# Kernel tuning notes

Hardware: AMD Instinct MI355X
Metric: run time of the kernel (lower is better)

The kernel has to match this reference:

```python
import jax, jax.numpy as jnp
import numpy as np

N = 50000      # areaNum
E = 64         # embeddingsize
NE = 800000    # nonzeros of normalized adjacency
WK = 9         # walk_length + 1
L = 2          # args.L
TMP = 0.5      # args.choosing_tmp
BIAS = 1e-4


def _logistic_noise(k, shape):
    # eps ~ U(bias, 1-bias); noise = log(eps) - log(1-eps)
    u = jax.random.uniform(k, shape, minval=BIAS, maxval=1.0 - BIAS)
    return jnp.log(u) - jnp.log1p(-u)


def setup_inputs() -> dict:
    key = jax.random.key(0)
    ks = jax.random.split(key, 16)
    rng = np.random.default_rng(0)

    # ---- normalized sparse adjacency (D^-1/2 A D^-1/2), COO sorted by row ----
    row = np.sort(rng.integers(0, N, NE))
    col = rng.integers(0, N, NE)
    deg = np.bincount(row, minlength=N).astype(np.float32)
    dinv = np.where(deg > 0, deg ** -0.5, 0.0).astype(np.float32)
    vals = dinv[row] * dinv[col]

    # ---- random-walk mean-pooling adjacency, row-normalized ----
    rw_row = np.repeat(np.arange(N), WK)
    rw_col = rng.integers(0, N, N * WK)
    rw_col[::WK] = np.arange(N)  # walk starts at self
    rw_vals = np.full(N * WK, 1.0 / WK, dtype=np.float32)

    def lin(k, fan_in, shape):
        return jax.random.normal(k, shape, dtype=jnp.float32) / np.sqrt(fan_in)

    inp = {
        'x': jax.random.normal(ks[0], (N, E), dtype=jnp.float32),
        'vals': jnp.asarray(vals),
        'rw_vals': jnp.asarray(rw_vals),
        't_W1': lin(ks[1], 2 * E, (L, 2 * E, E)),
        't_b1': jnp.zeros((L, E), jnp.float32),
        't_W2': lin(ks[2], E, (L, E, 1)),
        't_b2': jnp.zeros((L, 1), jnp.float32),
        's_W1': lin(ks[3], E, (L, E, E)),
        's_b1': jnp.zeros((L, E), jnp.float32),
        's_W2': lin(ks[4], E, (L, E, 1)),
        's_b2': jnp.zeros((L, 1), jnp.float32),
        't_noise': _logistic_noise(ks[5], (L, NE)),
        's_noise': _logistic_noise(ks[6], (L, N, 1)),
        'row': jnp.asarray(row, dtype=jnp.int64) if jax.config.jax_enable_x64 else jnp.asarray(row, dtype=jnp.int32),
        'col': jnp.asarray(col, dtype=jnp.int32),
        'rw_row': jnp.asarray(rw_row, dtype=jnp.int32),
        'rw_col': jnp.asarray(rw_col, dtype=jnp.int32),
    }
    inp['row'] = jnp.asarray(row, dtype=jnp.int32)
    return inp


def reference(x, vals, rw_vals, t_W1, t_b1, t_W2, t_b2, s_W1, s_b1, s_W2, s_b2,
              t_noise, s_noise, row, col, rw_row, rw_col):
    n = x.shape[0]

    def spmm(r, c, v, h):  # sparse [n,n] @ dense [n,E]
        return jax.ops.segment_sum(v[:, None] * h[c], r, num_segments=n)

    # per-edge concat of ORIGINAL embeddings (same tensor every layer, as in source)
    t_cat = jnp.concatenate([x[row], x[col]], axis=-1)  # [nE, 2E]

    # --- mask-learning pass ---
    cur = x
    t_masks, s_masks = [], []
    for i in range(L):
        cur = spmm(row, col, vals, cur)
        t_h = jax.nn.relu(t_cat @ t_W1[i] + t_b1[i])
        t_logit = t_h @ t_W2[i] + t_b2[i]                      # [nE,1]
        t_m = jax.nn.sigmoid((t_noise[i][:, None] + t_logit) / TMP)[:, 0]
        t_masks.append(t_m)
        s_h = jax.nn.relu(cur @ s_W1[i] + s_b1[i])
        s_logit = s_h @ s_W2[i] + s_b2[i]                      # [N,1]
        s_masks.append(jax.nn.sigmoid((s_noise[i] + s_logit) / TMP))

    # --- t branch: gated spmm propagation, mean over layers ---
    cur_t = x
    acc_t = x
    for i in range(L):
        cur_t = spmm(row, col, vals * t_masks[i], cur_t)
        acc_t = acc_t + cur_t
    emb_t = acc_t / (L + 1)

    # --- s branch: gated mix with random-walk mean pooling, then spmm ---
    cur_s = x
    acc_s = x
    s_reg = jnp.float32(0.0)
    for i in range(L):
        mp = spmm(rw_row, rw_col, rw_vals, cur_s)
        cur_s = s_masks[i] * cur_s + (1.0 - s_masks[i]) * mp
        cur_s = spmm(row, col, vals, cur_s)
        acc_s = acc_s + cur_s
        s_reg = s_reg + s_masks[i].sum() / n
    emb_s = acc_s / (L + 1)
    s_reg = s_reg / L
    t_reg = jnp.float32(0.0)  # source never accumulates into t_reg
    return emb_t, emb_s, t_reg, s_reg, t_masks[-1]
```

## Files before the change

### kernel.cpp

```cpp
#include <hip/hip_runtime.h>

#define NNODES 50000
#define EDIM 64
#define WKLEN 9
#define NEDGE 800000
#define NPAD (NNODES + 64)

#define NGRP 6250
#define GSTRIDE 1250

using bf16x8 = __attribute__((ext_vector_type(8))) __bf16;
using f32x4  = __attribute__((ext_vector_type(4))) float;

__device__ __align__(256) unsigned short g_xbf[NPAD * EDIM];
__device__ __align__(256) unsigned short g_ABh[NNODES * 128];
__device__ __align__(256) unsigned short g_c1h[NPAD * EDIM];
__device__ __align__(256) unsigned short g_c2h[NPAD * EDIM];
__device__ __align__(256) unsigned short g_g0h[NNODES * EDIM];
__device__ __align__(256) unsigned short g_sc1h[NNODES * EDIM];
__device__ __align__(256) unsigned short g_Pr[NNODES * 128];
__device__ __align__(256) unsigned short g_Pc[NNODES * 128];
__device__ __align__(256) float g_mt0[NEDGE];
__device__ __align__(256) float g_mt1[NEDGE];
__device__ __align__(256) float g_sm0[NNODES];
__device__ __align__(256) float g_sm1[NNODES];
__device__ __align__(256) int   g_rowptr[NNODES + 1];
__device__ __align__(256) unsigned short g_Tswz[2048 * 8];
__device__ __align__(256) unsigned short g_Sswz[1024 * 8];

__device__ __forceinline__ unsigned short f2bf(float f) {
    union { float f; unsigned int i; } v;
    v.f = f;
    unsigned int r = v.i + 0x7FFFu + ((v.i >> 16) & 1u);
    return (unsigned short)(r >> 16);
}
__device__ __forceinline__ float bf2f_lo(unsigned int u) {
    union { unsigned int i; float f; } v; v.i = u << 16; return v.f;
}
__device__ __forceinline__ float bf2f_hi(unsigned int u) {
    union { unsigned int i; float f; } v; v.i = u & 0xFFFF0000u; return v.f;
}

__global__ __launch_bounds__(256) void misc_kernel(
    const float* __restrict__ x, const float* __restrict__ tW1,
    const float* __restrict__ sW1, const int* __restrict__ row,
    int n, int nE)
{
    int bid = blockIdx.x, tid = threadIdx.x;
    if (bid < 1563) {
        int i = bid * 256 + tid;
        if (i < NNODES * EDIM / 8) {
            const float* src = x + i * 8;
            union { unsigned short s[8]; uint4 q; } u;
#pragma unroll
            for (int j = 0; j < 8; ++j) u.s[j] = f2bf(src[j]);
            *(uint4*)&g_xbf[i * 8] = u.q;
        }
    } else if (bid < 1759) {
        int i = (bid - 1563) * 256 + tid;
        if (i > n) return;
        int lo = 0, hi = nE;
        while (lo < hi) {
            int mid = (lo + hi) >> 1;
            if (row[mid] < i) lo = mid + 1; else hi = mid;
        }
        g_rowptr[i] = lo;
    } else if (bid < 1767) {
        int t = (bid - 1759) * 256 + tid;
        int s = t >> 9, f = (t >> 6) & 7, ln = t & 63;
        int li = s >> 1, half = s & 1, ks = f >> 2, nn = f & 3;
        int q = ln >> 4, mcl = ln & 15;
        union { unsigned short sv[8]; uint4 q4; } u;
#pragma unroll
        for (int j = 0; j < 8; ++j) {
            int kg = half * 64 + ks * 32 + q * 8 + j;
            u.sv[j] = f2bf(tW1[li * 8192 + kg * 64 + nn * 16 + mcl]);
        }
        *(uint4*)&g_Tswz[t * 8] = u.q4;
    } else {
        int t = (bid - 1767) * 256 + tid;
        int li = t >> 9, ks = (t >> 8) & 1, nn = (t >> 6) & 3, ln = t & 63;
        int q = ln >> 4, mcl = ln & 15;
        union { unsigned short sv[8]; uint4 q4; } u;
#pragma unroll
        for (int j = 0; j < 8; ++j)
            u.sv[j] = f2bf(sW1[li * 4096 + (ks * 32 + q * 8 + j) * 64 + nn * 16 + mcl]);
        *(uint4*)&g_Sswz[t * 8] = u.q4;
    }
}

__global__ __launch_bounds__(256) void prep2_kernel(int n)
{
    int tid = threadIdx.x;
    int wave = tid >> 6, lane = tid & 63;
    int mc = lane & 15, quad = lane >> 4;
    int nb = blockIdx.x * 64 + wave * 16;
    const unsigned short* bp = g_xbf + (nb + mc) * 64 + quad * 8;
    bf16x8 af0 = *(const bf16x8*)bp;
    bf16x8 af1 = *(const bf16x8*)(bp + 32);
    const f32x4 zero = {0.f, 0.f, 0.f, 0.f};
#pragma unroll
    for (int s = 0; s < 4; ++s) {
        int li = s >> 1, half = s & 1;
        f32x4 acc[4];
#pragma unroll
        for (int nn = 0; nn < 4; ++nn) acc[nn] = zero;
#pragma unroll
        for (int nn = 0; nn < 4; ++nn) {
            bf16x8 b0 = *(const bf16x8*)&g_Tswz[((s * 8 + nn) * 64 + lane) * 8];
            bf16x8 b1 = *(const bf16x8*)&g_Tswz[((s * 8 + 4 + nn) * 64 + lane) * 8];
            acc[nn] = __builtin_amdgcn_mfma_f32_16x16x32_bf16(af0, b0, acc[nn], 0, 0, 0);
            acc[nn] = __builtin_amdgcn_mfma_f32_16x16x32_bf16(af1, b1, acc[nn], 0, 0, 0);
        }
        unsigned short* dst = half ? g_Pc : g_Pr;
#pragma unroll
        for (int nn = 0; nn < 4; ++nn)
#pragma unroll
            for (int r = 0; r < 4; ++r) {
                int node = nb + quad * 4 + r;
                if (node < n)
                    dst[node * 128 + li * 64 + nn * 16 + mc] = f2bf(acc[nn][r]);
            }
    }
}

__global__ __launch_bounds__(256) void edge_mask_kernel(
    const float* __restrict__ tb1, const float* __restrict__ tW2,
    const float* __restrict__ tb2, const float* __restrict__ tnoise,
    const int* __restrict__ row, const int* __restrict__ col,
    float* __restrict__ mask_out, int nE)
{
    int tid = threadIdx.x;
    int lane = tid & 63;
    int sub = lane & 7;
    int eg = lane >> 3;

    float b1_0[8], b1_1[8], w2_0[8], w2_1[8];
    *(float4*)&b1_0[0] = *(const float4*)&tb1[sub * 8];
    *(float4*)&b1_0[4] = *(const float4*)&tb1[sub * 8 + 4];
    *(float4*)&b1_1[0] = *(const float4*)&tb1[64 + sub * 8];
    *(float4*)&b1_1[4] = *(const float4*)&tb1[64 + sub * 8 + 4];
    *(float4*)&w2_0[0] = *(const float4*)&tW2[sub * 8];
    *(float4*)&w2_0[4] = *(const float4*)&tW2[sub * 8 + 4];
    *(float4*)&w2_1[0] = *(const float4*)&tW2[64 + sub * 8];
    *(float4*)&w2_1[4] = *(const float4*)&tW2[64 + sub * 8 + 4];
    float tb2_0 = tb2[0], tb2_1 = tb2[1];

    int nvb = nE / 32;
    for (int vb = blockIdx.x; vb < nvb; vb += GSTRIDE) {
        int wv = vb * 4 + (tid >> 6);
        int e = wv * 8 + eg;

        int rn = row[e], cn = col[e];
        uint4 qr0 = *(const uint4*)&g_Pr[rn * 128 + sub * 8];
        uint4 qr1 = *(const uint4*)&g_Pr[rn * 128 + 64 + sub * 8];
        uint4 qc0 = *(const uint4*)&g_Pc[cn * 128 + sub * 8];
        uint4 qc1 = *(const uint4*)&g_Pc[cn * 128 + 64 + sub * 8];

        float p0 = 0.f, p1 = 0.f;
        unsigned r0[4] = {qr0.x, qr0.y, qr0.z, qr0.w};
        unsigned r1[4] = {qr1.x, qr1.y, qr1.z, qr1.w};
        unsigned c0[4] = {qc0.x, qc0.y, qc0.z, qc0.w};
        unsigned c1[4] = {qc1.x, qc1.y, qc1.z, qc1.w};
#pragma unroll
        for (int k = 0; k < 4; ++k) {
            float hA = fmaxf(bf2f_lo(r0[k]) + bf2f_lo(c0[k]) + b1_0[2 * k], 0.f);
            float hB = fmaxf(bf2f_hi(r0[k]) + bf2f_hi(c0[k]) + b1_0[2 * k + 1], 0.f);
            p0 = fmaf(hA, w2_0[2 * k], p0);
            p0 = fmaf(hB, w2_0[2 * k + 1], p0);
            float gA = fmaxf(bf2f_lo(r1[k]) + bf2f_lo(c1[k]) + b1_1[2 * k], 0.f);
            float gB = fmaxf(bf2f_hi(r1[k]) + bf2f_hi(c1[k]) + b1_1[2 * k + 1], 0.f);
            p1 = fmaf(gA, w2_1[2 * k], p1);
            p1 = fmaf(gB, w2_1[2 * k + 1], p1);
        }
#pragma unroll
        for (int off = 1; off <= 4; off <<= 1) {
            p0 += __shfl_xor(p0, off, 64);
            p1 += __shfl_xor(p1, off, 64);
        }
        if (sub == 0) {
            float z0 = (tnoise[e] + p0 + tb2_0) * 2.0f;
            float m0 = 1.0f / (1.0f + expf(-z0));
            g_mt0[e] = m0;
            float z1 = (tnoise[nE + e] + p1 + tb2_1) * 2.0f;
            float m1 = 1.0f / (1.0f + expf(-z1));
            g_mt1[e] = m1;
            mask_out[e] = m1;
        }
    }
}

__device__ __forceinline__ void nm_body(
    int bid, const unsigned short* __restrict__ cur, int li,
    const float* __restrict__ b1, const float* __restrict__ W2,
    const float* __restrict__ b2, const float* __restrict__ noise,
    float* __restrict__ smout, int n)
{
    int tid = threadIdx.x;
    int wave = tid >> 6, lane = tid & 63;
    int mc = lane & 15, quad = lane >> 4;
    int nb = bid * 64 + wave * 16;
    const unsigned short* basep = cur + (nb + mc) * 64 + quad * 8;
    bf16x8 af0 = *(const bf16x8*)basep;
    bf16x8 af1 = *(const bf16x8*)(basep + 32);
    f32x4 acc[4];
    const f32x4 zero = {0.f, 0.f, 0.f, 0.f};
#pragma unroll
    for (int nn = 0; nn < 4; ++nn) acc[nn] = zero;
#pragma unroll
    for (int nn = 0; nn < 4; ++nn) {
        bf16x8 b0 = *(const bf16x8*)&g_Sswz[((li * 8 + nn) * 64 + lane) * 8];
        bf16x8 b1f = *(const bf16x8*)&g_Sswz[((li * 8 + 4 + nn) * 64 + lane) * 8];
        acc[nn] = __builtin_amdgcn_mfma_f32_16x16x32_bf16(af0, b0, acc[nn], 0, 0, 0);
        acc[nn] = __builtin_amdgcn_mfma_f32_16x16x32_bf16(af1, b1f, acc[nn], 0, 0, 0);
    }
    float p[4];
#pragma unroll
    for (int r = 0; r < 4; ++r) {
        float s = 0.f;
#pragma unroll
        for (int nn = 0; nn < 4; ++nn) {
            float h = acc[nn][r] + b1[nn * 16 + mc];
            s = fmaf(fmaxf(h, 0.f), W2[nn * 16 + mc], s);
        }
        p[r] = s;
    }
#pragma unroll
    for (int off = 8; off >= 1; off >>= 1)
#pragma unroll
        for (int r = 0; r < 4; ++r) p[r] += __shfl_xor(p[r], off, 64);
    if (mc == 0) {
        float b2v = b2[0];
#pragma unroll
        for (int r = 0; r < 4; ++r) {
            int node = nb + quad * 4 + r;
            if (node < n) {
                float z = (noise[node] + p[r] + b2v) * 2.0f;
                smout[node] = 1.0f / (1.0f + expf(-z));
            }
        }
    }
}

__global__ __launch_bounds__(256) void nm0_kernel(
    const float* __restrict__ sb1, const float* __restrict__ sW2,
    const float* __restrict__ sb2, const float* __restrict__ snz, int n)
{
    nm_body(blockIdx.x, g_c1h, 0, sb1, sW2, sb2, snz, g_sm0, n);
}

__device__ __forceinline__ void s1_process16(
    int sb, int d2, int myc, float myv, float myvm,
    float& p0, float& p1, float& q0, float& q1)
{
    int cc[16]; float vv[16], mm[16]; unsigned uu[16];
#pragma unroll
    for (int k = 0; k < 16; ++k) {
        cc[k] = __shfl(myc, sb + k, 64);
        vv[k] = __shfl(myv, sb + k, 64);
        mm[k] = __shfl(myvm, sb + k, 64);
    }
#pragma unroll
    for (int k = 0; k < 16; ++k)
        uu[k] = *(const unsigned*)&g_xbf[cc[k] * 64 + 2 * d2];
#pragma unroll
    for (int k = 0; k < 16; ++k) {
        p0 = fmaf(vv[k], bf2f_lo(uu[k]), p0);
        p1 = fmaf(vv[k], bf2f_hi(uu[k]), p1);
        q0 = fmaf(mm[k], bf2f_lo(uu[k]), q0);
        q1 = fmaf(mm[k], bf2f_hi(uu[k]), q1);
    }
}

__global__ __launch_bounds__(256) void s1_kernel(
    const int* __restrict__ colv, const float* __restrict__ vals, int n)
{
    int half = threadIdx.x >> 5;
    int el = half & 1;
    int d2 = threadIdx.x & 31;
    int sb0 = el << 5;
    for (int rb = blockIdx.x; rb < NGRP; rb += GSTRIDE) {
        int w = rb * 8 + half;
        int s = g_rowptr[w], e = g_rowptr[w + 1];
        float p0 = 0.f, p1 = 0.f, q0 = 0.f, q1 = 0.f;
        for (int base = s; base < e; base += 32) {
            int rem = e - base;
            int myc = 0; float myv = 0.f, myvm = 0.f;
            if (d2 < rem) {
                myc = colv[base + d2];
                myv = vals[base + d2];
                myvm = myv * g_mt0[base + d2];
            }
            s1_process16(sb0, d2, myc, myv, myvm, p0, p1, q0, q1);
            if (rem > 16)
                s1_process16(sb0 + 16, d2, myc, myv, myvm, p0, p1, q0, q1);
        }
        uint2 pk;
        pk.x = (unsigned)f2bf(p0) | ((unsigned)f2bf(q0) << 16);
        pk.y = (unsigned)f2bf(p1) | ((unsigned)f2bf(q1) << 16);
        *(uint2*)&g_ABh[w * 128 + 4 * d2] = pk;
        *(unsigned*)&g_c1h[w * 64 + 2 * d2] =
            (unsigned)f2bf(p0) | ((unsigned)f2bf(p1) << 16);
    }
}

__device__ __forceinline__ void s2_process8(
    int sb, int d2, int myc, float myv, float myvm,
    float& c0, float& c1, float& t0, float& t1)
{
    int cc[8]; float vv[8], mm[8]; uint2 uu[8];
#pragma unroll
    for (int k = 0; k < 8; ++k) {
        cc[k] = __shfl(myc, sb + k, 64);
        vv[k] = __shfl(myv, sb + k, 64);
        mm[k] = __shfl(myvm, sb + k, 64);
    }
#pragma unroll
    for (int k = 0; k < 8; ++k)
        uu[k] = *(const uint2*)&g_ABh[cc[k] * 128 + 4 * d2];
#pragma unroll
    for (int k = 0; k < 8; ++k) {
        c0 = fmaf(vv[k], bf2f_lo(uu[k].x), c0);
        t0 = fmaf(mm[k], bf2f_hi(uu[k].x), t0);
        c1 = fmaf(vv[k], bf2f_lo(uu[k].y), c1);
        t1 = fmaf(mm[k], bf2f_hi(uu[k].y), t1);
    }
}

__device__ __forceinline__ void rw_body(
    int bid, const int* __restrict__ rw_col, const float* __restrict__ rwv,
    const unsigned short* __restrict__ cur, const float* __restrict__ smask,
    unsigned short* __restrict__ outg)
{
    int w = bid * 8 + (threadIdx.x >> 5);
    int d2 = threadIdx.x & 31;
    int base = w * WKLEN;
    float a0 = 0.f, a1 = 0.f;
#pragma unroll
    for (int j = 0; j < WKLEN; ++j) {
        int c = rw_col[base + j];
        float v = rwv[base + j];
        unsigned u = *(const unsigned*)&cur[c * 64 + 2 * d2];
        a0 = fmaf(v, bf2f_lo(u), a0);
        a1 = fmaf(v, bf2f_hi(u), a1);
    }
    float sm = smask[w];
    unsigned u = *(const unsigned*)&cur[w * 64 + 2 * d2];
    float r0 = sm * bf2f_lo(u) + (1.f - sm) * a0;
    float r1 = sm * bf2f_hi(u) + (1.f - sm) * a1;
    *(unsigned*)&outg[w * 64 + 2 * d2] =
        (unsigned)f2bf(r0) | ((unsigned)f2bf(r1) << 16);
}

__global__ __launch_bounds__(256) void s2_rw0_kernel(
    const int* __restrict__ colv, const float* __restrict__ vals,
    const int* __restrict__ rw_col, const float* __restrict__ rwv,
    const float* __restrict__ x, float* __restrict__ emb_t, int n)
{
    int half = threadIdx.x >> 5;
    int el = half & 1;
    int d2 = threadIdx.x & 31;
    int sb0 = el << 5;
    for (int vb = blockIdx.x; vb < 2 * NGRP; vb += GSTRIDE) {
        if (vb >= NGRP) {
            rw_body(vb - NGRP, rw_col, rwv, g_xbf, g_sm0, g_g0h);
            continue;
        }
        int w = vb * 8 + half;
        int s = g_rowptr[w], e = g_rowptr[w + 1];
        float c0 = 0.f, c1 = 0.f, t0 = 0.f, t1 = 0.f;
        for (int base = s; base < e; base += 32) {
            int rem = e - base;
            int myc = 0; float myv = 0.f, myvm = 0.f;
            if (d2 < rem) {
                myc = colv[base + d2];
                myv = vals[base + d2];
                myvm = myv * g_mt1[base + d2];
            }
            s2_process8(sb0, d2, myc, myv, myvm, c0, c1, t0, t1);
            if (rem > 8)  s2_process8(sb0 + 8,  d2, myc, myv, myvm, c0, c1, t0, t1);
            if (rem > 16) s2_process8(sb0 + 16, d2, myc, myv, myvm, c0, c1, t0, t1);
            if (rem > 24) s2_process8(sb0 + 24, d2, myc, myv, myvm, c0, c1, t0, t1);
        }
        int o2 = w * 64 + 2 * d2;
        uint2 U2v = *(const uint2*)&g_ABh[w * 128 + 4 * d2];
        float2 et;
        et.x = (x[o2]     + bf2f_hi(U2v.x) + t0) * (1.0f / 3.0f);
        et.y = (x[o2 + 1] + bf2f_hi(U2v.y) + t1) * (1.0f / 3.0f);
        *(float2*)&emb_t[o2] = et;
        *(unsigned*)&g_c2h[o2] = (unsigned)f2bf(c0) | ((unsigned)f2bf(c1) << 16);
    }
}

__device__ __forceinline__ void sp_process16(
    const unsigned short* __restrict__ h, int sb, int d2,
    int myc, float myv, float& a0, float& a1)
{
    int cc[16]; float vv[16]; unsigned uu[16];
#pragma unroll
    for (int k = 0; k < 16; ++k) {
        cc[k] = __shfl(myc, sb + k, 64);
        vv[k] = __shfl(myv, sb + k, 64);
    }
#pragma unroll
    for (int k = 0; k < 16; ++k)
        uu[k] = *(const unsigned*)&h[cc[k] * 64 + 2 * d2];
#pragma unroll
    for (int k = 0; k < 16; ++k) {
        a0 = fmaf(vv[k], bf2f_lo(uu[k]), a0);
        a1 = fmaf(vv[k], bf2f_hi(uu[k]), a1);
    }
}

__device__ __forceinline__ void spmm_body(
    int bid, const int* __restrict__ colv, const float* __restrict__ vals,
    const unsigned short* __restrict__ h, float* __restrict__ l0,
    float* __restrict__ l1, int* __restrict__ wout, int* __restrict__ d2out)
{
    int half = threadIdx.x >> 5;
    int w = bid * 8 + half;
    int el = half & 1;
    int d2 = threadIdx.x & 31;
    int sb0 = el << 5;
    int s = g_rowptr[w], e = g_rowptr[w + 1];
    float a0 = 0.f, a1 = 0.f;
    for (int base = s; base < e; base += 32) {
        int rem = e - base;
        int myc = 0; float myv = 0.f;
        if (d2 < rem) {
            myc = colv[base + d2];
            myv = vals[base + d2];
        }
        sp_process16(h, sb0, d2, myc, myv, a0, a1);
        if (rem > 16) sp_process16(h, sb0 + 16, d2, myc, myv, a0, a1);
    }
    *l0 = a0; *l1 = a1; *wout = w; *d2out = d2;
}

__global__ __launch_bounds__(256) void spmm10_nm1_kernel(
    const int* __restrict__ colv, const float* __restrict__ vals,
    const float* __restrict__ sb1, const float* __restrict__ sW2,
    const float* __restrict__ sb2, const float* __restrict__ snz, int n)
{
    for (int vb = blockIdx.x; vb < NGRP + 782; vb += GSTRIDE) {
        if (vb >= NGRP) {
            nm_body(vb - NGRP, g_c2h, 1, sb1, sW2, sb2, snz, g_sm1, n);
            continue;
        }
        float a0, a1; int w, d2;
        spmm_body(vb, colv, vals, g_g0h, &a0, &a1, &w, &d2);
        *(unsigned*)&g_sc1h[w * 64 + 2 * d2] =
            (unsigned)f2bf(a0) | ((unsigned)f2bf(a1) << 16);
    }
}

__global__ __launch_bounds__(256) void rw1_kernel(
    const int* __restrict__ rw_col, const float* __restrict__ rwv)
{
    for (int vb = blockIdx.x; vb < NGRP; vb += GSTRIDE)
        rw_body(vb, rw_col, rwv, g_sc1h, g_sm1, g_g0h);
}

__global__ __launch_bounds__(256) void spmm12_fin_kernel(
    const int* __restrict__ colv, const float* __restrict__ vals,
    const float* __restrict__ x, float* __restrict__ emb_s,
    float* __restrict__ out, int n)
{
    if (blockIdx.x >= GSTRIDE) {
        __shared__ float red[256];
        float s = 0.f;
        for (int i = threadIdx.x; i < n; i += 256) s += g_sm0[i] + g_sm1[i];
        red[threadIdx.x] = s;
        __syncthreads();
        for (int off = 128; off >= 1; off >>= 1) {
            if (threadIdx.x < off) red[threadIdx.x] += red[threadIdx.x + off];
            __syncthreads();
        }
        if (threadIdx.x == 0) {
            out[6400000] = 0.0f;
            out[6400001] = red[0] / (2.0f * n);
        }
        return;
    }
    for (int vb = blockIdx.x; vb < NGRP; vb += GSTRIDE) {
        float a0, a1; int w, d2;
        spmm_body(vb, colv, vals, g_g0h, &a0, &a1, &w, &d2);
        int o2 = w * 64 + 2 * d2;
        unsigned uc = *(const unsigned*)&g_sc1h[o2];
        float2 es;
        es.x = (x[o2]     + bf2f_lo(uc) + a0) * (1.0f / 3.0f);
        es.y = (x[o2 + 1] + bf2f_hi(uc) + a1) * (1.0f / 3.0f);
        *(float2*)&emb_s[o2] = es;
    }
}

extern "C" void kernel_launch(void* const* d_in, const int* in_sizes, int n_in,
                              void* d_out, int out_size, void* d_ws, size_t ws_size,
                              hipStream_t stream)
{
    const float* x    = (const float*)d_in[0];
    const float* vals = (const float*)d_in[1];
    const float* rwv  = (const float*)d_in[2];
    const float* tW1  = (const float*)d_in[3];
    const float* tb1  = (const float*)d_in[4];
    const float* tW2  = (const float*)d_in[5];
    const float* tb2  = (const float*)d_in[6];
    const float* sW1  = (const float*)d_in[7];
    const float* sb1  = (const float*)d_in[8];
    const float* sW2  = (const float*)d_in[9];
    const float* sb2  = (const float*)d_in[10];
    const float* tnz  = (const float*)d_in[11];
    const float* snz  = (const float*)d_in[12];
    const int* row   = (const int*)d_in[13];
    const int* colv  = (const int*)d_in[14];
    const int* rwcol = (const int*)d_in[16];

    const int n = NNODES;
    const int nE = in_sizes[1];

    float* out   = (float*)d_out;
    float* emb_t = out;
    float* emb_s = out + 3200000;
    float* masko = out + 6400002;

    misc_kernel<<<1771, 256, 0, stream>>>(x, tW1, sW1, row, n, nE);
    prep2_kernel<<<782, 256, 0, stream>>>(n);
    edge_mask_kernel<<<GSTRIDE, 256, 0, stream>>>(tb1, tW2, tb2, tnz,
                                                  row, colv, masko, nE);
    s1_kernel<<<GSTRIDE, 256, 0, stream>>>(colv, vals, n);
    nm0_kernel<<<782, 256, 0, stream>>>(sb1, sW2, sb2, snz, n);
    s2_rw0_kernel<<<GSTRIDE, 256, 0, stream>>>(colv, vals, rwcol, rwv, x, emb_t, n);
    spmm10_nm1_kernel<<<GSTRIDE, 256, 0, stream>>>(colv, vals,
                                                   sb1 + 64, sW2 + 64, sb2 + 1,
                                                   snz + n, n);
    rw1_kernel<<<GSTRIDE, 256, 0, stream>>>(rwcol, rwv);
    spmm12_fin_kernel<<<GSTRIDE + 1, 256, 0, stream>>>(colv, vals, x, emb_s, out, n);
}
```

Before: 346.0 us.

## Remap sparse kernels to 16 lanes per row with wider vector gathers

Each row is now handled by 16 lanes instead of 32, and each lane covers 4 feature columns (8 in the packed pass) using uint2/uint4 loads. Before, edge indices were loaded once per lane and then broadcast with shuffles. Now every lane loads the edge indices and values directly, in unrolled batches of 16. Grid sizes change to match the new row grouping. The aim is fewer shuffle instructions and fewer, wider gather transactions per row, at the cost of redundant index loads and higher register pressure.

```diff
diff --git a/kernel.cpp b/kernel.cpp
--- a/kernel.cpp
+++ b/kernel.cpp
@@ -6,7 +6,9 @@
 #define NEDGE 800000
 #define NPAD (NNODES + 64)
 
-#define NGRP 6250
+#define NG16 3125
+#define GS1 1563
+#define GS2 1303
 #define GSTRIDE 1250
 
 using bf16x8 = __attribute__((ext_vector_type(8))) __bf16;
@@ -249,107 +251,89 @@
     nm_body(blockIdx.x, g_c1h, 0, sb1, sW2, sb2, snz, g_sm0, n);
 }
 
-__device__ __forceinline__ void s1_process16(
-    int sb, int d2, int myc, float myv, float myvm,
-    float& p0, float& p1, float& q0, float& q1)
-{
-    int cc[16]; float vv[16], mm[16]; unsigned uu[16];
-#pragma unroll
-    for (int k = 0; k < 16; ++k) {
-        cc[k] = __shfl(myc, sb + k, 64);
-        vv[k] = __shfl(myv, sb + k, 64);
-        mm[k] = __shfl(myvm, sb + k, 64);
-    }
-#pragma unroll
-    for (int k = 0; k < 16; ++k)
-        uu[k] = *(const unsigned*)&g_xbf[cc[k] * 64 + 2 * d2];
-#pragma unroll
-    for (int k = 0; k < 16; ++k) {
-        p0 = fmaf(vv[k], bf2f_lo(uu[k]), p0);
-        p1 = fmaf(vv[k], bf2f_hi(uu[k]), p1);
-        q0 = fmaf(mm[k], bf2f_lo(uu[k]), q0);
-        q1 = fmaf(mm[k], bf2f_hi(uu[k]), q1);
-    }
-}
-
 __global__ __launch_bounds__(256) void s1_kernel(
     const int* __restrict__ colv, const float* __restrict__ vals, int n)
 {
-    int half = threadIdx.x >> 5;
-    int el = half & 1;
-    int d2 = threadIdx.x & 31;
-    int sb0 = el << 5;
-    for (int rb = blockIdx.x; rb < NGRP; rb += GSTRIDE) {
-        int w = rb * 8 + half;
+    int g = threadIdx.x >> 4;
+    int l = threadIdx.x & 15;
+    for (int vb = blockIdx.x; vb < NG16; vb += GS1) {
+        int w = vb * 16 + g;
         int s = g_rowptr[w], e = g_rowptr[w + 1];
-        float p0 = 0.f, p1 = 0.f, q0 = 0.f, q1 = 0.f;
-        for (int base = s; base < e; base += 32) {
-            int rem = e - base;
-            int myc = 0; float myv = 0.f, myvm = 0.f;
-            if (d2 < rem) {
-                myc = colv[base + d2];
-                myv = vals[base + d2];
-                myvm = myv * g_mt0[base + d2];
+        float p0 = 0.f, p1 = 0.f, p2 = 0.f, p3 = 0.f;
+        float q0 = 0.f, q1 = 0.f, q2 = 0.f, q3 = 0.f;
+        for (int base = s; base < e; base += 16) {
+            int cc[16]; float vv[16], mm[16];
+#pragma unroll
+            for (int k = 0; k < 16; ++k) {
+                int idx = base + k;
+                bool ok = idx < e;
+                cc[k] = ok ? colv[idx] : 0;
+                float v = ok ? vals[idx] : 0.f;
+                vv[k] = v;
+                mm[k] = ok ? v * g_mt0[idx] : 0.f;
             }
-            s1_process16(sb0, d2, myc, myv, myvm, p0, p1, q0, q1);
-            if (rem > 16)
-                s1_process16(sb0 + 16, d2, myc, myv, myvm, p0, p1, q0, q1);
-        }
-        uint2 pk;
+            uint2 uu[16];
+#pragma unroll
+            for (int k = 0; k < 16; ++k)
+                uu[k] = *(const uint2*)&g_xbf[cc[k] * 64 + 4 * l];
+#pragma unroll
+            for (int k = 0; k < 16; ++k) {
+                p0 = fmaf(vv[k], bf2f_lo(uu[k].x), p0);
+                p1 = fmaf(vv[k], bf2f_hi(uu[k].x), p1);
+                p2 = fmaf(vv[k], bf2f_lo(uu[k].y), p2);
+                p3 = fmaf(vv[k], bf2f_hi(uu[k].y), p3);
+                q0 = fmaf(mm[k], bf2f_lo(uu[k].x), q0);
+                q1 = fmaf(mm[k], bf2f_hi(uu[k].x), q1);
+                q2 = fmaf(mm[k], bf2f_lo(uu[k].y), q2);
+                q3 = fmaf(mm[k], bf2f_hi(uu[k].y), q3);
+            }
+        }
+        uint4 pk;
         pk.x = (unsigned)f2bf(p0) | ((unsigned)f2bf(q0) << 16);
         pk.y = (unsigned)f2bf(p1) | ((unsigned)f2bf(q1) << 16);
-        *(uint2*)&g_ABh[w * 128 + 4 * d2] = pk;
-        *(unsigned*)&g_c1h[w * 64 + 2 * d2] =
-            (unsigned)f2bf(p0) | ((unsigned)f2bf(p1) << 16);
-    }
-}
-
-__device__ __forceinline__ void s2_process8(
-    int sb, int d2, int myc, float myv, float myvm,
-    float& c0, float& c1, float& t0, float& t1)
-{
-    int cc[8]; float vv[8], mm[8]; uint2 uu[8];
-#pragma unroll
-    for (int k = 0; k < 8; ++k) {
-        cc[k] = __shfl(myc, sb + k, 64);
-        vv[k] = __shfl(myv, sb + k, 64);
-        mm[k] = __shfl(myvm, sb + k, 64);
-    }
-#pragma unroll
-    for (int k = 0; k < 8; ++k)
-        uu[k] = *(const uint2*)&g_ABh[cc[k] * 128 + 4 * d2];
-#pragma unroll
-    for (int k = 0; k < 8; ++k) {
-        c0 = fmaf(vv[k], bf2f_lo(uu[k].x), c0);
-        t0 = fmaf(mm[k], bf2f_hi(uu[k].x), t0);
-        c1 = fmaf(vv[k], bf2f_lo(uu[k].y), c1);
-        t1 = fmaf(mm[k], bf2f_hi(uu[k].y), t1);
-    }
-}
-
-__device__ __forceinline__ void rw_body(
+        pk.z = (unsigned)f2bf(p2) | ((unsigned)f2bf(q2) << 16);
+        pk.w = (unsigned)f2bf(p3) | ((unsigned)f2bf(q3) << 16);
+        *(uint4*)&g_ABh[w * 128 + 8 * l] = pk;
+        uint2 ch;
+        ch.x = (unsigned)f2bf(p0) | ((unsigned)f2bf(p1) << 16);
+        ch.y = (unsigned)f2bf(p2) | ((unsigned)f2bf(p3) << 16);
+        *(uint2*)&g_c1h[w * 64 + 4 * l] = ch;
+    }
+}
+
+__device__ __forceinline__ void rw_body16(
     int bid, const int* __restrict__ rw_col, const float* __restrict__ rwv,
     const unsigned short* __restrict__ cur, const float* __restrict__ smask,
     unsigned short* __restrict__ outg)
 {
-    int w = bid * 8 + (threadIdx.x >> 5);
-    int d2 = threadIdx.x & 31;
+    int g = threadIdx.x >> 4, l = threadIdx.x & 15;
+    int w = bid * 16 + g;
     int base = w * WKLEN;
-    float a0 = 0.f, a1 = 0.f;
+    int cc[WKLEN]; float vv[WKLEN];
 #pragma unroll
     for (int j = 0; j < WKLEN; ++j) {
-        int c = rw_col[base + j];
-        float v = rwv[base + j];
-        unsigned u = *(const unsigned*)&cur[c * 64 + 2 * d2];
-        a0 = fmaf(v, bf2f_lo(u), a0);
-        a1 = fmaf(v, bf2f_hi(u), a1);
+        cc[j] = rw_col[base + j];
+        vv[j] = rwv[base + j];
+    }
+    float a0 = 0.f, a1 = 0.f, a2 = 0.f, a3 = 0.f;
+#pragma unroll
+    for (int j = 0; j < WKLEN; ++j) {
+        uint2 u = *(const uint2*)&cur[cc[j] * 64 + 4 * l];
+        a0 = fmaf(vv[j], bf2f_lo(u.x), a0);
+        a1 = fmaf(vv[j], bf2f_hi(u.x), a1);
+        a2 = fmaf(vv[j], bf2f_lo(u.y), a2);
+        a3 = fmaf(vv[j], bf2f_hi(u.y), a3);
     }
     float sm = smask[w];
-    unsigned u = *(const unsigned*)&cur[w * 64 + 2 * d2];
-    float r0 = sm * bf2f_lo(u) + (1.f - sm) * a0;
-    float r1 = sm * bf2f_hi(u) + (1.f - sm) * a1;
-    *(unsigned*)&outg[w * 64 + 2 * d2] =
-        (unsigned)f2bf(r0) | ((unsigned)f2bf(r1) << 16);
+    uint2 u = *(const uint2*)&cur[w * 64 + 4 * l];
+    float r0 = sm * bf2f_lo(u.x) + (1.f - sm) * a0;
+    float r1 = sm * bf2f_hi(u.x) + (1.f - sm) * a1;
+    float r2 = sm * bf2f_lo(u.y) + (1.f - sm) * a2;
+    float r3 = sm * bf2f_hi(u.y) + (1.f - sm) * a3;
+    uint2 o;
+    o.x = (unsigned)f2bf(r0) | ((unsigned)f2bf(r1) << 16);
+    o.y = (unsigned)f2bf(r2) | ((unsigned)f2bf(r3) << 16);
+    *(uint2*)&outg[w * 64 + 4 * l] = o;
 }
 
 __global__ __launch_bounds__(256) void s2_rw0_kernel(
@@ -357,84 +341,97 @@
     const int* __restrict__ rw_col, const float* __restrict__ rwv,
     const float* __restrict__ x, float* __restrict__ emb_t, int n)
 {
-    int half = threadIdx.x >> 5;
-    int el = half & 1;
-    int d2 = threadIdx.x & 31;
-    int sb0 = el << 5;
-    for (int vb = blockIdx.x; vb < 2 * NGRP; vb += GSTRIDE) {
-        if (vb >= NGRP) {
-            rw_body(vb - NGRP, rw_col, rwv, g_xbf, g_sm0, g_g0h);
+    int g = threadIdx.x >> 4;
+    int l = threadIdx.x & 15;
+    for (int vb = blockIdx.x; vb < 2 * NG16; vb += GS1) {
+        if (vb >= NG16) {
+            rw_body16(vb - NG16, rw_col, rwv, g_xbf, g_sm0, g_g0h);
             continue;
         }
-        int w = vb * 8 + half;
+        int w = vb * 16 + g;
         int s = g_rowptr[w], e = g_rowptr[w + 1];
-        float c0 = 0.f, c1 = 0.f, t0 = 0.f, t1 = 0.f;
-        for (int base = s; base < e; base += 32) {
-            int rem = e - base;
-            int myc = 0; float myv = 0.f, myvm = 0.f;
-            if (d2 < rem) {
-                myc = colv[base + d2];
-                myv = vals[base + d2];
-                myvm = myv * g_mt1[base + d2];
+        float c0 = 0.f, c1 = 0.f, c2 = 0.f, c3 = 0.f;
+        float t0 = 0.f, t1 = 0.f, t2 = 0.f, t3 = 0.f;
+        for (int base = s; base < e; base += 16) {
+            int cc[16]; float vv[16], mm[16];
+#pragma unroll
+            for (int k = 0; k < 16; ++k) {
+                int idx = base + k;
+                bool ok = idx < e;
+                cc[k] = ok ? colv[idx] : 0;
+                float v = ok ? vals[idx] : 0.f;
+                vv[k] = v;
+                mm[k] = ok ? v * g_mt1[idx] : 0.f;
             }
-            s2_process8(sb0, d2, myc, myv, myvm, c0, c1, t0, t1);
-            if (rem > 8)  s2_process8(sb0 + 8,  d2, myc, myv, myvm, c0, c1, t0, t1);
-            if (rem > 16) s2_process8(sb0 + 16, d2, myc, myv, myvm, c0, c1, t0, t1);
-            if (rem > 24) s2_process8(sb0 + 24, d2, myc, myv, myvm, c0, c1, t0, t1);
-        }
-        int o2 = w * 64 + 2 * d2;
-        uint2 U2v = *(const uint2*)&g_ABh[w * 128 + 4 * d2];
-        float2 et;
-        et.x = (x[o2]     + bf2f_hi(U2v.x) + t0) * (1.0f / 3.0f);
-        et.y = (x[o2 + 1] + bf2f_hi(U2v.y) + t1) * (1.0f / 3.0f);
-        *(float2*)&emb_t[o2] = et;
-        *(unsigned*)&g_c2h[o2] = (unsigned)f2bf(c0) | ((unsigned)f2bf(c1) << 16);
-    }
-}
-
-__device__ __forceinline__ void sp_process16(
-    const unsigned short* __restrict__ h, int sb, int d2,
-    int myc, float myv, float& a0, float& a1)
-{
-    int cc[16]; float vv[16]; unsigned uu[16];
-#pragma unroll
-    for (int k = 0; k < 16; ++k) {
-        cc[k] = __shfl(myc, sb + k, 64);
-        vv[k] = __shfl(myv, sb + k, 64);
-    }
-#pragma unroll
-    for (int k = 0; k < 16; ++k)
-        uu[k] = *(const unsigned*)&h[cc[k] * 64 + 2 * d2];
-#pragma unroll
-    for (int k = 0; k < 16; ++k) {
-        a0 = fmaf(vv[k], bf2f_lo(uu[k]), a0);
-        a1 = fmaf(vv[k], bf2f_hi(uu[k]), a1);
-    }
-}
-
-__device__ __forceinline__ void spmm_body(
-    int bid, const int* __restrict__ colv, const float* __restrict__ vals,
-    const unsigned short* __restrict__ h, float* __restrict__ l0,
-    float* __restrict__ l1, int* __restrict__ wout, int* __restrict__ d2out)
-{
-    int half = threadIdx.x >> 5;
-    int w = bid * 8 + half;
-    int el = half & 1;
-    int d2 = threadIdx.x & 31;
-    int sb0 = el << 5;
+#pragma unroll
+            for (int h = 0; h < 2; ++h) {
+                if (h == 1 && e - base <= 8) break;
+                uint4 uu[8];
+#pragma unroll
+                for (int k = 0; k < 8; ++k)
+                    uu[k] = *(const uint4*)&g_ABh[cc[h * 8 + k] * 128 + 8 * l];
+#pragma unroll
+                for (int k = 0; k < 8; ++k) {
+                    float v = vv[h * 8 + k], m = mm[h * 8 + k];
+                    c0 = fmaf(v, bf2f_lo(uu[k].x), c0);
+                    t0 = fmaf(m, bf2f_hi(uu[k].x), t0);
+                    c1 = fmaf(v, bf2f_lo(uu[k].y), c1);
+                    t1 = fmaf(m, bf2f_hi(uu[k].y), t1);
+                    c2 = fmaf(v, bf2f_lo(uu[k].z), c2);
+                    t2 = fmaf(m, bf2f_hi(uu[k].z), t2);
+                    c3 = fmaf(v, bf2f_lo(uu[k].w), c3);
+                    t3 = fmaf(m, bf2f_hi(uu[k].w), t3);
+                }
+            }
+        }
+        int o = w * 64 + 4 * l;
+        uint4 U = *(const uint4*)&g_ABh[w * 128 + 8 * l];
+        float4 xv = *(const float4*)&x[o];
+        float4 et;
+        et.x = (xv.x + bf2f_hi(U.x) + t0) * (1.0f / 3.0f);
+        et.y = (xv.y + bf2f_hi(U.y) + t1) * (1.0f / 3.0f);
+        et.z = (xv.z + bf2f_hi(U.z) + t2) * (1.0f / 3.0f);
+        et.w = (xv.w + bf2f_hi(U.w) + t3) * (1.0f / 3.0f);
+        *(float4*)&emb_t[o] = et;
+        uint2 ch;
+        ch.x = (unsigned)f2bf(c0) | ((unsigned)f2bf(c1) << 16);
+        ch.y = (unsigned)f2bf(c2) | ((unsigned)f2bf(c3) << 16);
+        *(uint2*)&g_c2h[o] = ch;
+    }
+}
+
+__device__ __forceinline__ void spmm_body16(
+    int vb, const int* __restrict__ colv, const float* __restrict__ vals,
+    const unsigned short* __restrict__ h,
+    float& a0, float& a1, float& a2, float& a3, int& wout, int& lout)
+{
+    int g = threadIdx.x >> 4;
+    int l = threadIdx.x & 15;
+    int w = vb * 16 + g;
     int s = g_rowptr[w], e = g_rowptr[w + 1];
-    float a0 = 0.f, a1 = 0.f;
-    for (int base = s; base < e; base += 32) {
-        int rem = e - base;
-        int myc = 0; float myv = 0.f;
-        if (d2 < rem) {
-            myc = colv[base + d2];
-            myv = vals[base + d2];
-        }
-        sp_process16(h, sb0, d2, myc, myv, a0, a1);
-        if (rem > 16) sp_process16(h, sb0 + 16, d2, myc, myv, a0, a1);
-    }
-    *l0 = a0; *l1 = a1; *wout = w; *d2out = d2;
+    a0 = a1 = a2 = a3 = 0.f;
+    for (int base = s; base < e; base += 16) {
+        int cc[16]; float vv[16];
+#pragma unroll
+        for (int k = 0; k < 16; ++k) {
+            int idx = base + k;
+            bool ok = idx < e;
+            cc[k] = ok ? colv[idx] : 0;
+            vv[k] = ok ? vals[idx] : 0.f;
+        }
+        uint2 uu[16];
+#pragma unroll
+        for (int k = 0; k < 16; ++k)
+            uu[k] = *(const uint2*)&h[cc[k] * 64 + 4 * l];
+#pragma unroll
+        for (int k = 0; k < 16; ++k) {
+            a0 = fmaf(vv[k], bf2f_lo(uu[k].x), a0);
+            a1 = fmaf(vv[k], bf2f_hi(uu[k].x), a1);
+            a2 = fmaf(vv[k], bf2f_lo(uu[k].y), a2);
+            a3 = fmaf(vv[k], bf2f_hi(uu[k].y), a3);
+        }
+    }
+    wout = w; lout = l;
 }
 
 __global__ __launch_bounds__(256) void spmm10_nm1_kernel(
@@ -442,23 +439,25 @@
     const float* __restrict__ sb1, const float* __restrict__ sW2,
     const float* __restrict__ sb2, const float* __restrict__ snz, int n)
 {
-    for (int vb = blockIdx.x; vb < NGRP + 782; vb += GSTRIDE) {
-        if (vb >= NGRP) {
-            nm_body(vb - NGRP, g_c2h, 1, sb1, sW2, sb2, snz, g_sm1, n);
+    for (int vb = blockIdx.x; vb < NG16 + 782; vb += GS2) {
+        if (vb >= NG16) {
+            nm_body(vb - NG16, g_c2h, 1, sb1, sW2, sb2, snz, g_sm1, n);
             continue;
         }
-        float a0, a1; int w, d2;
-        spmm_body(vb, colv, vals, g_g0h, &a0, &a1, &w, &d2);
-        *(unsigned*)&g_sc1h[w * 64 + 2 * d2] =
-            (unsigned)f2bf(a0) | ((unsigned)f2bf(a1) << 16);
+        float a0, a1, a2, a3; int w, l;
+        spmm_body16(vb, colv, vals, g_g0h, a0, a1, a2, a3, w, l);
+        uint2 ch;
+        ch.x = (unsigned)f2bf(a0) | ((unsigned)f2bf(a1) << 16);
+        ch.y = (unsigned)f2bf(a2) | ((unsigned)f2bf(a3) << 16);
+        *(uint2*)&g_sc1h[w * 64 + 4 * l] = ch;
     }
 }
 
 __global__ __launch_bounds__(256) void rw1_kernel(
     const int* __restrict__ rw_col, const float* __restrict__ rwv)
 {
-    for (int vb = blockIdx.x; vb < NGRP; vb += GSTRIDE)
-        rw_body(vb, rw_col, rwv, g_sc1h, g_sm1, g_g0h);
+    for (int vb = blockIdx.x; vb < NG16; vb += GS1)
+        rw_body16(vb, rw_col, rwv, g_sc1h, g_sm1, g_g0h);
 }
 
 __global__ __launch_bounds__(256) void spmm12_fin_kernel(
@@ -466,7 +465,7 @@
     const float* __restrict__ x, float* __restrict__ emb_s,
     float* __restrict__ out, int n)
 {
-    if (blockIdx.x >= GSTRIDE) {
+    if (blockIdx.x >= GS1) {
         __shared__ float red[256];
         float s = 0.f;
         for (int i = threadIdx.x; i < n; i += 256) s += g_sm0[i] + g_sm1[i];
@@ -482,15 +481,18 @@
         }
         return;
     }
-    for (int vb = blockIdx.x; vb < NGRP; vb += GSTRIDE) {
-        float a0, a1; int w, d2;
-        spmm_body(vb, colv, vals, g_g0h, &a0, &a1, &w, &d2);
-        int o2 = w * 64 + 2 * d2;
-        unsigned uc = *(const unsigned*)&g_sc1h[o2];
-        float2 es;
-        es.x = (x[o2]     + bf2f_lo(uc) + a0) * (1.0f / 3.0f);
-        es.y = (x[o2 + 1] + bf2f_hi(uc) + a1) * (1.0f / 3.0f);
-        *(float2*)&emb_s[o2] = es;
+    for (int vb = blockIdx.x; vb < NG16; vb += GS1) {
+        float a0, a1, a2, a3; int w, l;
+        spmm_body16(vb, colv, vals, g_g0h, a0, a1, a2, a3, w, l);
+        int o = w * 64 + 4 * l;
+        uint2 uc = *(const uint2*)&g_sc1h[o];
+        float4 xv = *(const float4*)&x[o];
+        float4 es;
+        es.x = (xv.x + bf2f_lo(uc.x) + a0) * (1.0f / 3.0f);
+        es.y = (xv.y + bf2f_hi(uc.x) + a1) * (1.0f / 3.0f);
+        es.z = (xv.z + bf2f_lo(uc.y) + a2) * (1.0f / 3.0f);
+        es.w = (xv.w + bf2f_hi(uc.y) + a3) * (1.0f / 3.0f);
+        *(float4*)&emb_s[o] = es;
     }
 }
 
@@ -527,12 +529,12 @@
     prep2_kernel<<<782, 256, 0, stream>>>(n);
     edge_mask_kernel<<<GSTRIDE, 256, 0, stream>>>(tb1, tW2, tb2, tnz,
                                                   row, colv, masko, nE);
-    s1_kernel<<<GSTRIDE, 256, 0, stream>>>(colv, vals, n);
+    s1_kernel<<<GS1, 256, 0, stream>>>(colv, vals, n);
     nm0_kernel<<<782, 256, 0, stream>>>(sb1, sW2, sb2, snz, n);
-    s2_rw0_kernel<<<GSTRIDE, 256, 0, stream>>>(colv, vals, rwcol, rwv, x, emb_t, n);
-    spmm10_nm1_kernel<<<GSTRIDE, 256, 0, stream>>>(colv, vals,
-                                                   sb1 + 64, sW2 + 64, sb2 + 1,
-                                                   snz + n, n);
-    rw1_kernel<<<GSTRIDE, 256, 0, stream>>>(rwcol, rwv);
-    spmm12_fin_kernel<<<GSTRIDE + 1, 256, 0, stream>>>(colv, vals, x, emb_s, out, n);
-}
+    s2_rw0_kernel<<<GS1, 256, 0, stream>>>(colv, vals, rwcol, rwv, x, emb_t, n);
+    spmm10_nm1_kernel<<<GS2, 256, 0, stream>>>(colv, vals,
+                                               sb1 + 64, sW2 + 64, sb2 + 1,
+                                               snz + n, n);
+    rw1_kernel<<<GS1, 256, 0, stream>>>(rwcol, rwv);
+    spmm12_fin_kernel<<<GS1 + 1, 256, 0, stream>>>(colv, vals, x, emb_s, out, n);
+}
```

Result: slower. 411.2 us (+18.8%).
